# Kernel optimization log

Hardware: AMD Instinct MI355X
Metric: run time of the kernel (lower is better)

## Reference

```python
import jax, jax.numpy as jnp
import numpy as np

F_NUM, KW, EMB = 256, 2, 300


def _conv_pool(X, W, b):
    # X: [B, L, E]; W: [F, kw, E]; b: [F]. Conv2d over [kw, E] window (full embedding
    # width) -> [B, F, T], ReLU, then AvgPool over the full T -> [B, F].
    kw = W.shape[1]
    T = X.shape[1] - kw + 1
    Xs = jnp.stack([X[:, k:k + T, :] for k in range(kw)], axis=1)  # [B, kw, T, E]
    y = jnp.einsum('fke,bkte->bft', W, Xs) + b[None, :, None]
    return jax.nn.relu(y).mean(axis=2)


def _unit(v):
    return v / jnp.sqrt((v * v).sum(-1, keepdims=True))


def setup_inputs() -> dict:
    key = jax.random.key(0)
    ks = jax.random.split(key, 20)
    wscale = 1.0 / np.sqrt(KW * EMB)
    inp = {
        'mention_vec': jax.random.normal(ks[0], (256, 10, 300), jnp.float32),
        'context_vec': jax.random.normal(ks[1], (256, 20, 300), jnp.float32),
        'doc_vec': jax.random.normal(ks[2], (200, 300), jnp.float32),
        'title_vec': jax.random.normal(ks[3], (1024, 20, 300), jnp.float32),
        'body_vec': jax.random.normal(ks[4], (1024, 200, 300), jnp.float32),
        'W_ms': jax.random.normal(ks[5], (F_NUM, KW, EMB), jnp.float32) * wscale,
        'b_ms': jax.random.normal(ks[6], (F_NUM,), jnp.float32) * wscale,
        'W_mc': jax.random.normal(ks[7], (F_NUM, KW, EMB), jnp.float32) * wscale,
        'b_mc': jax.random.normal(ks[8], (F_NUM,), jnp.float32) * wscale,
        'W_md': jax.random.normal(ks[9], (F_NUM, KW, EMB), jnp.float32) * wscale,
        'b_md': jax.random.normal(ks[10], (F_NUM,), jnp.float32) * wscale,
        'W_et': jax.random.normal(ks[11], (F_NUM, KW, EMB), jnp.float32) * wscale,
        'b_et': jax.random.normal(ks[12], (F_NUM,), jnp.float32) * wscale,
        'W_eb': jax.random.normal(ks[13], (F_NUM, KW, EMB), jnp.float32) * wscale,
        'b_eb': jax.random.normal(ks[14], (F_NUM,), jnp.float32) * wscale,
        'w_local': jax.random.normal(ks[15], (6,), jnp.float32) * 0.1,
        'b_local': jax.random.normal(ks[16], (1,), jnp.float32) * 0.1,
        'mention_entity': jax.random.randint(ks[17], (256, 1024), 0, 2, jnp.int32),
    }
    return inp


def reference(mention_vec, context_vec, doc_vec, title_vec, body_vec,
              W_ms, b_ms, W_mc, b_mc, W_md, b_md, W_et, b_et, W_eb, b_eb,
              w_local, b_local, mention_entity):
    # Per-branch conv + relu + avg-pool feature extraction -> [*, F] vectors.
    ms = _conv_pool(mention_vec, W_ms, b_ms)        # [m, F]
    mc = _conv_pool(context_vec, W_mc, b_mc)        # [m, F]
    md = _conv_pool(doc_vec[None], W_md, b_md)[0]   # [F]
    et = _conv_pool(title_vec, W_et, b_et)          # [n, F]
    eb = _conv_pool(body_vec, W_eb, b_eb)           # [n, F]

    nms, nmc, net, neb, nmd = _unit(ms), _unit(mc), _unit(et), _unit(eb), _unit(md)
    cos_st = nms @ net.T                             # [m, n]
    cos_ct = nmc @ net.T
    cos_sb = nms @ neb.T
    cos_cb = nmc @ neb.T
    cos_dt = jnp.broadcast_to((net @ nmd)[None, :], cos_st.shape)
    cos_db = jnp.broadcast_to((neb @ nmd)[None, :], cos_st.shape)

    # cos(x,y)/2 + 0.5, but features are exactly 0 where mention_entity == 0.
    feats = jnp.stack([cos_st, cos_dt, cos_ct, cos_sb, cos_db, cos_cb], axis=-1)
    feats = feats / 2.0 + 0.5                        # [m, n, 6]
    mask = mention_entity.astype(feats.dtype)
    feats = feats * mask[:, :, None]

    score = feats @ w_local + b_local[0]             # [m, n] (tiny 6->1 linear)
    score = score * mask

    # masked softmax with temperature 0.1 (e**(x/0.1) * mask, row-normalized)
    e = jnp.exp(score / 0.1) * mask
    norm = e / e.sum(axis=1, keepdims=True)
    return score, norm
```

## Files before the change

kernel.cpp:

```cpp
#include <hip/hip_runtime.h>
#include <math.h>

typedef __bf16 bf16_t;
typedef __bf16 bf16x4 __attribute__((ext_vector_type(4)));
typedef __bf16 bf16x8 __attribute__((ext_vector_type(8)));
typedef float  f32x4  __attribute__((ext_vector_type(4)));

#define FNUM 256
#define KPAD 608
#define NKS  19

__global__ __launch_bounds__(256)
void prep_w_swz(const float* __restrict__ w0, const float* __restrict__ w1,
                const float* __restrict__ w2, const float* __restrict__ w3,
                const float* __restrict__ w4, bf16_t* __restrict__ wp) {
    int tg = blockIdx.x * 4 + (threadIdx.x >> 6);
    if (tg >= 1520) return;
    int l  = threadIdx.x & 63;
    int br = tg / 304;
    int rem = tg % 304;
    int ks = rem / 16, ft = rem % 16;
    const float* src;
    switch (br) {
        case 0: src = w0; break;
        case 1: src = w1; break;
        case 2: src = w2; break;
        case 3: src = w3; break;
        default: src = w4; break;
    }
    int f = ft * 16 + (l & 15);
    int k0 = ks * 32 + (l >> 4) * 8;
    bf16x8 v;
#pragma unroll
    for (int e = 0; e < 8; e++) {
        int k = k0 + e;
        v[e] = (k < 600) ? (bf16_t)src[(size_t)f * 600 + k] : (bf16_t)0.f;
    }
    *(bf16x8*)(wp + (size_t)br * FNUM * KPAD + ((size_t)(ks * 16 + ft) * 512 + (size_t)l * 8)) = v;
}

__global__ __launch_bounds__(512, 4)
void conv_body(const float* __restrict__ X, const bf16_t* __restrict__ Wswz,
               const float* __restrict__ bias, float* __restrict__ part,
               const float* __restrict__ X2, const bf16_t* __restrict__ W2,
               const float* __restrict__ bias2) {
    constexpr int NFRAG = 8;
    constexpr int TT    = 128;
    constexpr int NROWS = TT + 1;
    __shared__ bf16_t Xlds[NROWS * 300 + 8];

    const int tid = threadIdx.x;
    const int l   = tid & 63;
    const int w   = tid >> 6;
    const int g   = l >> 4;
    const int l15 = l & 15;

    const float* Xb;
    const bf16_t* Wb;
    const float* bp;
    int slot, t0;
    if ((int)blockIdx.x >= 2048) {
        int c = blockIdx.x - 2048;
        Xb = X2; Wb = W2; bp = bias2;
        slot = 2048 + c;
        t0 = c * TT;
    } else {
        int batch = blockIdx.x >> 1;
        int c = blockIdx.x & 1;
        Xb = X + (size_t)batch * 60000;
        Wb = Wswz; bp = bias;
        slot = batch * 2 + c;
        t0 = c * TT;
    }

    {
        const int vr  = (200 - t0 < NROWS) ? (200 - t0) : NROWS;
        const float* src = Xb + (size_t)t0 * 300;
        const int nF4 = vr * 75;
        for (int v = tid; v < nF4; v += 512) {
            float4 fv = *(const float4*)(src + (size_t)v * 4);
            bf16x4 hv = { (bf16_t)fv.x, (bf16_t)fv.y, (bf16_t)fv.z, (bf16_t)fv.w };
            *(bf16x4*)(Xlds + v * 4) = hv;
        }
        bf16x4 z4 = { (bf16_t)0.f, (bf16_t)0.f, (bf16_t)0.f, (bf16_t)0.f };
        for (int v = nF4 + tid; v < NROWS * 75; v += 512)
            *(bf16x4*)(Xlds + v * 4) = z4;
        if (tid < 4) ((unsigned int*)(Xlds + NROWS * 300))[tid] = 0u;
    }

    const bf16_t* wa = Wb + ((size_t)(2 * w) * 512 + (size_t)l * 8);

    int boff[NFRAG];
#pragma unroll
    for (int j = 0; j < NFRAG; j++)
        boff[j] = (j * 16 + l15) * 300 + g * 8;

    bf16x8 aCur[2], aNxt[2];
#pragma unroll
    for (int i = 0; i < 2; i++) aCur[i] = *(const bf16x8*)(wa + i * 512);

    __syncthreads();

    f32x4 acc[2][NFRAG];
#pragma unroll
    for (int i = 0; i < 2; i++)
#pragma unroll
        for (int j = 0; j < NFRAG; j++)
            acc[i][j] = (f32x4){0.f, 0.f, 0.f, 0.f};

    for (int ks = 0; ks < NKS; ++ks) {
        if (ks + 1 < NKS) {
            const bf16_t* wn_p = wa + (size_t)(ks + 1) * 16 * 512;
#pragma unroll
            for (int i = 0; i < 2; i++) aNxt[i] = *(const bf16x8*)(wn_p + i * 512);
        }
        const int k0 = ks * 32;
        bf16x8 bb[NFRAG];
#pragma unroll
        for (int j = 0; j < NFRAG; j++) {
            bf16x4 lo = *(const bf16x4*)(Xlds + boff[j] + k0);
            bf16x4 hi = *(const bf16x4*)(Xlds + boff[j] + k0 + 4);
            bb[j] = __builtin_shufflevector(lo, hi, 0, 1, 2, 3, 4, 5, 6, 7);
        }
#pragma unroll
        for (int i = 0; i < 2; i++)
#pragma unroll
            for (int j = 0; j < NFRAG; j++)
                acc[i][j] = __builtin_amdgcn_mfma_f32_16x16x32_bf16(aCur[i], bb[j], acc[i][j], 0, 0, 0);
#pragma unroll
        for (int i = 0; i < 2; i++) aCur[i] = aNxt[i];
    }

#pragma unroll
    for (int i = 0; i < 2; i++) {
#pragma unroll
        for (int r = 0; r < 4; r++) {
            const int row = w * 32 + i * 16 + g * 4 + r;
            const float bi = bp[row];
            float s = 0.f;
#pragma unroll
            for (int j = 0; j < NFRAG; j++) {
                int t = t0 + j * 16 + l15;
                float v = acc[i][j][r] + bi;
                v = fmaxf(v, 0.f);
                s += (t < 199) ? v : 0.f;
            }
            s += __shfl_xor(s, 1);
            s += __shfl_xor(s, 2);
            s += __shfl_xor(s, 4);
            s += __shfl_xor(s, 8);
            if (l15 == 0) part[(size_t)slot * 256 + row] = s;
        }
    }
}

__global__ __launch_bounds__(256)
void combine_norm(const float* __restrict__ part, float* __restrict__ nebT,
                  float* __restrict__ nmd) {
    __shared__ float red[4];
    int bid = blockIdx.x, tid = threadIdx.x;
    float v = part[((size_t)bid * 2 + 0) * 256 + tid]
            + part[((size_t)bid * 2 + 1) * 256 + tid];
    float sq = v * v;
    sq += __shfl_xor(sq, 1);
    sq += __shfl_xor(sq, 2);
    sq += __shfl_xor(sq, 4);
    sq += __shfl_xor(sq, 8);
    sq += __shfl_xor(sq, 16);
    sq += __shfl_xor(sq, 32);
    if ((tid & 63) == 0) red[tid >> 6] = sq;
    __syncthreads();
    float tot = red[0] + red[1] + red[2] + red[3];
    float o = v / sqrtf(tot);
    if (bid >= 1024) nmd[tid] = o;
    else             nebT[(size_t)tid * 1024 + bid] = o;
}

template<int NF>
__device__ __forceinline__ void kloop_s(const bf16_t* __restrict__ wa,
        const bf16_t* __restrict__ buf, f32x4 (&acc)[2][NF], const int (&boff)[NF]) {
    bf16x8 aCur[2], aNxt[2];
    aCur[0] = *(const bf16x8*)(wa);
    aCur[1] = *(const bf16x8*)(wa + 512);
#pragma unroll
    for (int ks = 0; ks < NKS; ++ks) {
        if (ks + 1 < NKS) {
            const bf16_t* wn = wa + (size_t)(ks + 1) * (16 * 512);
            aNxt[0] = *(const bf16x8*)(wn);
            aNxt[1] = *(const bf16x8*)(wn + 512);
        }
        const int k0 = ks * 32;
#pragma unroll
        for (int j = 0; j < NF; ++j) {
            const bf16_t* p = buf + boff[j] + k0;
            bf16x4 lo = *(const bf16x4*)(p);
            bf16x4 hi = *(const bf16x4*)(p + 4);
            bf16x8 bb = __builtin_shufflevector(lo, hi, 0, 1, 2, 3, 4, 5, 6, 7);
            acc[0][j] = __builtin_amdgcn_mfma_f32_16x16x32_bf16(aCur[0], bb, acc[0][j], 0, 0, 0);
            acc[1][j] = __builtin_amdgcn_mfma_f32_16x16x32_bf16(aCur[1], bb, acc[1][j], 0, 0, 0);
        }
        aCur[0] = aNxt[0]; aCur[1] = aNxt[1];
    }
}

template<int NFB, int L, int T, int BSTR, int ARRE>
__global__ __launch_bounds__(512, 4)
void conv_small(const float* __restrict__ XA, const bf16_t* __restrict__ WA,
                const float* __restrict__ bA, float* __restrict__ outA,
                const float* __restrict__ XB, const bf16_t* __restrict__ WB,
                const float* __restrict__ bB, float* __restrict__ outB,
                int nABlocks) {
    constexpr int NTOT = 4 * NFB;
    __shared__ bf16_t Xs[ARRE];
    __shared__ float feat4[4][256];

    const int tid = threadIdx.x, l = tid & 63, w = tid >> 6, g = l >> 4, l15 = l & 15;
    const bool modeA = ((int)blockIdx.x < nABlocks);
    const int grp = modeA ? (int)blockIdx.x : ((int)blockIdx.x - nABlocks);
    const int batch0 = grp * 4;
    const float* Xsrc = modeA ? XA : XB;
    const bf16_t* Wb = modeA ? WA : WB;
    const float* bp = modeA ? bA : bB;

#pragma unroll
    for (int b = 0; b < 4; ++b) {
        const float4* s4 = (const float4*)(Xsrc + (size_t)(batch0 + b) * (L * 300));
        for (int v = tid; v < L * 75; v += 512) {
            float4 f = s4[v];
            bf16x4 h = { (bf16_t)f.x, (bf16_t)f.y, (bf16_t)f.z, (bf16_t)f.w };
            *(bf16x4*)(Xs + b * BSTR + v * 4) = h;
        }
        if (tid < 2) {
            bf16x4 z = { (bf16_t)0.f, (bf16_t)0.f, (bf16_t)0.f, (bf16_t)0.f };
            *(bf16x4*)(Xs + b * BSTR + L * 300 + tid * 4) = z;
        }
    }
    __syncthreads();

    int boff[NTOT];
#pragma unroll
    for (int j = 0; j < NTOT; ++j)
        boff[j] = (j / NFB) * BSTR + ((j % NFB) * 16 + l15) * 300 + g * 8;

    f32x4 acc[2][NTOT];
#pragma unroll
    for (int a = 0; a < 2; a++)
#pragma unroll
        for (int j = 0; j < NTOT; j++) acc[a][j] = (f32x4){0.f, 0.f, 0.f, 0.f};

    const bf16_t* wa = Wb + (size_t)(2 * w) * 512 + (size_t)l * 8;
    kloop_s<NTOT>(wa, Xs, acc, boff);

#pragma unroll
    for (int jb = 0; jb < 4; ++jb) {
#pragma unroll
        for (int a = 0; a < 2; a++)
#pragma unroll
            for (int r = 0; r < 4; r++) {
                const float bi = bp[32 * w + a * 16 + g * 4 + r];
                float s = 0.f;
#pragma unroll
                for (int jf = 0; jf < NFB; ++jf) {
                    int t = jf * 16 + l15;
                    float v = acc[a][jb * NFB + jf][r] + bi;
                    v = fmaxf(v, 0.f);
                    s += (t < T) ? v : 0.f;
                }
                s += __shfl_xor(s, 1);
                s += __shfl_xor(s, 2);
                s += __shfl_xor(s, 4);
                s += __shfl_xor(s, 8);
                if (l15 == 0) feat4[jb][32 * w + a * 16 + g * 4 + r] = s;
            }
    }
    __syncthreads();

    if (w < 4) {
        float vv[4];
        float sq = 0.f;
#pragma unroll
        for (int q = 0; q < 4; q++) { vv[q] = feat4[w][l * 4 + q]; sq += vv[q] * vv[q]; }
        sq += __shfl_xor(sq, 1);
        sq += __shfl_xor(sq, 2);
        sq += __shfl_xor(sq, 4);
        sq += __shfl_xor(sq, 8);
        sq += __shfl_xor(sq, 16);
        sq += __shfl_xor(sq, 32);
        float rsq = 1.f / sqrtf(sq);
        int batch = batch0 + w;
        if (modeA) {
#pragma unroll
            for (int q = 0; q < 4; q++)
                outA[(size_t)(l * 4 + q) * 1024 + batch] = vv[q] * rsq;
        } else {
            float4 o = { vv[0] * rsq, vv[1] * rsq, vv[2] * rsq, vv[3] * rsq };
            *(float4*)(outB + (size_t)batch * 256 + l * 4) = o;
        }
    }
}

__global__ __launch_bounds__(256)
void dt_db_kernel(const float* __restrict__ nmd, const float* __restrict__ netT,
                  const float* __restrict__ nebT, float* __restrict__ dt,
                  float* __restrict__ db) {
    __shared__ float md[256];
    int tid = threadIdx.x;
    md[tid] = nmd[tid];
    __syncthreads();
    int n = blockIdx.x * 256 + tid;
    float dT = 0.f, dB = 0.f;
    for (int k = 0; k < 256; ++k) {
        float mk = md[k];
        dT += mk * netT[(size_t)k * 1024 + n];
        dB += mk * nebT[(size_t)k * 1024 + n];
    }
    dt[n] = dT;
    db[n] = dB;
}

__global__ __launch_bounds__(256)
void pair1(const float* __restrict__ nms, const float* __restrict__ nmc,
           const float* __restrict__ netT, const float* __restrict__ nebT,
           const float* __restrict__ dt, const float* __restrict__ db,
           const float* __restrict__ wl, const float* __restrict__ bl,
           const int* __restrict__ me, float* __restrict__ out,
           float* __restrict__ epart) {
    __shared__ float sA[4 * 256], sB[4 * 256];
    const int tid = threadIdx.x;
    const int mt = blockIdx.x >> 2;
    const int nt = blockIdx.x & 3;
    const int m0 = mt * 4, n0 = nt * 256;
    for (int v = tid; v < 1024; v += 256) {
        sA[v] = nms[(size_t)m0 * 256 + v];
        sB[v] = nmc[(size_t)m0 * 256 + v];
    }
    __syncthreads();
    const int ws = tid >> 6;
    const int nl = tid & 63;
    const int n  = n0 + nl * 4;
    const int m  = m0 + ws;

    float dst[4] = {0,0,0,0}, dct[4] = {0,0,0,0}, dsb[4] = {0,0,0,0}, dcb[4] = {0,0,0,0};
    for (int k = 0; k < 256; ++k) {
        float4 tv = *(const float4*)(netT + (size_t)k * 1024 + n);
        float4 bv = *(const float4*)(nebT + (size_t)k * 1024 + n);
        float a = sA[ws * 256 + k];
        float c = sB[ws * 256 + k];
        dst[0] += a * tv.x; dst[1] += a * tv.y; dst[2] += a * tv.z; dst[3] += a * tv.w;
        dct[0] += c * tv.x; dct[1] += c * tv.y; dct[2] += c * tv.z; dct[3] += c * tv.w;
        dsb[0] += a * bv.x; dsb[1] += a * bv.y; dsb[2] += a * bv.z; dsb[3] += a * bv.w;
        dcb[0] += c * bv.x; dcb[1] += c * bv.y; dcb[2] += c * bv.z; dcb[3] += c * bv.w;
    }

    float w0 = wl[0], w1 = wl[1], w2 = wl[2], w3 = wl[3], w4 = wl[4], w5 = wl[5], b = bl[0];
    float dtq[4], dbq[4];
    *(float4*)dtq = *(const float4*)(dt + n);
    *(float4*)dbq = *(const float4*)(db + n);
    const int* mp = me + (size_t)m * 1024 + n;
    float scv[4], evv[4];
    float esum = 0.f;
#pragma unroll
    for (int q = 0; q < 4; q++) {
        float msk = (float)mp[q];
        float f_st = dst[q] * 0.5f + 0.5f;
        float f_dt = dtq[q] * 0.5f + 0.5f;
        float f_ct = dct[q] * 0.5f + 0.5f;
        float f_sb = dsb[q] * 0.5f + 0.5f;
        float f_db = dbq[q] * 0.5f + 0.5f;
        float f_cb = dcb[q] * 0.5f + 0.5f;
        float s = f_st * w0 + f_dt * w1 + f_ct * w2 + f_sb * w3 + f_db * w4 + f_cb * w5 + b;
        s = (msk != 0.f) ? s : 0.f;
        scv[q] = s;
        evv[q] = (msk != 0.f) ? expf(s / 0.1f) : 0.f;
        esum += evv[q];
    }
    esum += __shfl_xor(esum, 1);
    esum += __shfl_xor(esum, 2);
    esum += __shfl_xor(esum, 4);
    esum += __shfl_xor(esum, 8);
    esum += __shfl_xor(esum, 16);
    esum += __shfl_xor(esum, 32);
    if (nl == 0) epart[(size_t)m * 4 + nt] = esum;

    *(float4*)(out + (size_t)m * 1024 + n) = *(float4*)scv;
    *(float4*)(out + 262144 + (size_t)m * 1024 + n) = *(float4*)evv;
}

__global__ __launch_bounds__(256)
void pair2(const float* __restrict__ epart, float* __restrict__ out2) {
    int m = blockIdx.x, tid = threadIdx.x;
    float tot = epart[(size_t)m * 4 + 0] + epart[(size_t)m * 4 + 1]
              + epart[(size_t)m * 4 + 2] + epart[(size_t)m * 4 + 3];
    float inv = 1.f / tot;
#pragma unroll
    for (int q = 0; q < 4; q++)
        out2[(size_t)m * 1024 + q * 256 + tid] *= inv;
}

extern "C" void kernel_launch(void* const* d_in, const int* in_sizes, int n_in,
                              void* d_out, int out_size, void* d_ws, size_t ws_size,
                              hipStream_t stream) {
    const float* mention = (const float*)d_in[0];
    const float* context = (const float*)d_in[1];
    const float* doc     = (const float*)d_in[2];
    const float* title   = (const float*)d_in[3];
    const float* body    = (const float*)d_in[4];
    const float* W_ms = (const float*)d_in[5];  const float* b_ms = (const float*)d_in[6];
    const float* W_mc = (const float*)d_in[7];  const float* b_mc = (const float*)d_in[8];
    const float* W_md = (const float*)d_in[9];  const float* b_md = (const float*)d_in[10];
    const float* W_et = (const float*)d_in[11]; const float* b_et = (const float*)d_in[12];
    const float* W_eb = (const float*)d_in[13]; const float* b_eb = (const float*)d_in[14];
    const float* w_local = (const float*)d_in[15];
    const float* b_local = (const float*)d_in[16];
    const int*   me      = (const int*)d_in[17];
    float* out = (float*)d_out;

    char* ws = (char*)d_ws;
    bf16_t* Wp = (bf16_t*)ws;
    size_t off = (size_t)5 * FNUM * KPAD * 2;
    float* part = (float*)(ws + off); off += (size_t)1025 * 2 * 256 * 4;
    float* nms  = (float*)(ws + off); off += 256 * 256 * 4;
    float* nmc  = (float*)(ws + off); off += 256 * 256 * 4;
    float* netT = (float*)(ws + off); off += 1024 * 256 * 4;
    float* nebT = (float*)(ws + off); off += 1024 * 256 * 4;
    float* nmd  = (float*)(ws + off); off += 256 * 4;
    float* dt   = (float*)(ws + off); off += 1024 * 4;
    float* db   = (float*)(ws + off); off += 1024 * 4;
    float* epart= (float*)(ws + off); off += 256 * 4 * 4;

    const bf16_t* Wms = Wp + (size_t)0 * FNUM * KPAD;
    const bf16_t* Wmc = Wp + (size_t)1 * FNUM * KPAD;
    const bf16_t* Wmd = Wp + (size_t)2 * FNUM * KPAD;
    const bf16_t* Wet = Wp + (size_t)3 * FNUM * KPAD;
    const bf16_t* Web = Wp + (size_t)4 * FNUM * KPAD;

    prep_w_swz<<<380, 256, 0, stream>>>(W_ms, W_mc, W_md, W_et, W_eb, Wp);

    conv_body<<<2050, 512, 0, stream>>>(body, Web, b_eb, part, doc, Wmd, b_md);

    conv_small<2, 20, 19, 6016, 27968><<<320, 512, 0, stream>>>(
        title, Wet, b_et, netT, context, Wmc, b_mc, nmc, 256);
    conv_small<1, 10, 9, 5120, 20480><<<64, 512, 0, stream>>>(
        mention, Wms, b_ms, netT, mention, Wms, b_ms, nms, 0);

    combine_norm<<<1025, 256, 0, stream>>>(part, nebT, nmd);
    dt_db_kernel<<<4, 256, 0, stream>>>(nmd, netT, nebT, dt, db);
    pair1<<<256, 256, 0, stream>>>(nms, nmc, netT, nebT, dt, db, w_local, b_local, me, out, epart);
    pair2<<<256, 256, 0, stream>>>(epart, out + 262144);
}
```

Measured before the change: 240.3 us.

## Fuse doc-cosine dot products into pair kernel and batch body loads

Removes the separate dt_db kernel and computes the doc-title and doc-body dot products inside pair1's existing k-loop, reusing the already-loaded netT/nebT vectors. This drops one launch and a small, poorly parallel kernel, at the cost of redundant recomputation across the m-tiles. The conv_body X staging loop now issues four float4 loads before converting, giving more memory-level parallelism. Pooled results go through shared memory so the partial sums are written with one coalesced store.

```diff
diff --git a/kernel.cpp b/kernel.cpp
--- a/kernel.cpp
+++ b/kernel.cpp
@@ -48,6 +48,7 @@
     constexpr int TT    = 128;
     constexpr int NROWS = TT + 1;
     __shared__ bf16_t Xlds[NROWS * 300 + 8];
+    __shared__ float  feat[256];
 
     const int tid = threadIdx.x;
     const int l   = tid & 63;
@@ -75,12 +76,23 @@
 
     {
         const int vr  = (200 - t0 < NROWS) ? (200 - t0) : NROWS;
-        const float* src = Xb + (size_t)t0 * 300;
+        const float4* s4 = (const float4*)(Xb + (size_t)t0 * 300);
         const int nF4 = vr * 75;
-        for (int v = tid; v < nF4; v += 512) {
-            float4 fv = *(const float4*)(src + (size_t)v * 4);
-            bf16x4 hv = { (bf16_t)fv.x, (bf16_t)fv.y, (bf16_t)fv.z, (bf16_t)fv.w };
-            *(bf16x4*)(Xlds + v * 4) = hv;
+        for (int v0 = tid; v0 < nF4; v0 += 512 * 4) {
+            float4 t[4];
+#pragma unroll
+            for (int q = 0; q < 4; ++q) {
+                int v = v0 + q * 512;
+                if (v < nF4) t[q] = s4[v];
+            }
+#pragma unroll
+            for (int q = 0; q < 4; ++q) {
+                int v = v0 + q * 512;
+                if (v < nF4) {
+                    bf16x4 hv = { (bf16_t)t[q].x, (bf16_t)t[q].y, (bf16_t)t[q].z, (bf16_t)t[q].w };
+                    *(bf16x4*)(Xlds + v * 4) = hv;
+                }
+            }
         }
         bf16x4 z4 = { (bf16_t)0.f, (bf16_t)0.f, (bf16_t)0.f, (bf16_t)0.f };
         for (int v = nF4 + tid; v < NROWS * 75; v += 512)
@@ -149,9 +161,12 @@
             s += __shfl_xor(s, 2);
             s += __shfl_xor(s, 4);
             s += __shfl_xor(s, 8);
-            if (l15 == 0) part[(size_t)slot * 256 + row] = s;
-        }
-    }
+            if (l15 == 0) feat[row] = s;
+        }
+    }
+    __syncthreads();
+    if (tid < 256)
+        part[(size_t)slot * 256 + tid] = feat[tid];
 }
 
 __global__ __launch_bounds__(256)
@@ -300,32 +315,13 @@
 }
 
 __global__ __launch_bounds__(256)
-void dt_db_kernel(const float* __restrict__ nmd, const float* __restrict__ netT,
-                  const float* __restrict__ nebT, float* __restrict__ dt,
-                  float* __restrict__ db) {
-    __shared__ float md[256];
-    int tid = threadIdx.x;
-    md[tid] = nmd[tid];
-    __syncthreads();
-    int n = blockIdx.x * 256 + tid;
-    float dT = 0.f, dB = 0.f;
-    for (int k = 0; k < 256; ++k) {
-        float mk = md[k];
-        dT += mk * netT[(size_t)k * 1024 + n];
-        dB += mk * nebT[(size_t)k * 1024 + n];
-    }
-    dt[n] = dT;
-    db[n] = dB;
-}
-
-__global__ __launch_bounds__(256)
 void pair1(const float* __restrict__ nms, const float* __restrict__ nmc,
            const float* __restrict__ netT, const float* __restrict__ nebT,
-           const float* __restrict__ dt, const float* __restrict__ db,
+           const float* __restrict__ nmd,
            const float* __restrict__ wl, const float* __restrict__ bl,
            const int* __restrict__ me, float* __restrict__ out,
            float* __restrict__ epart) {
-    __shared__ float sA[4 * 256], sB[4 * 256];
+    __shared__ float sA[4 * 256], sB[4 * 256], md[256];
     const int tid = threadIdx.x;
     const int mt = blockIdx.x >> 2;
     const int nt = blockIdx.x & 3;
@@ -334,6 +330,7 @@
         sA[v] = nms[(size_t)m0 * 256 + v];
         sB[v] = nmc[(size_t)m0 * 256 + v];
     }
+    md[tid] = nmd[tid];
     __syncthreads();
     const int ws = tid >> 6;
     const int nl = tid & 63;
@@ -341,21 +338,22 @@
     const int m  = m0 + ws;
 
     float dst[4] = {0,0,0,0}, dct[4] = {0,0,0,0}, dsb[4] = {0,0,0,0}, dcb[4] = {0,0,0,0};
+    float dtq[4] = {0,0,0,0}, dbq[4] = {0,0,0,0};
     for (int k = 0; k < 256; ++k) {
         float4 tv = *(const float4*)(netT + (size_t)k * 1024 + n);
         float4 bv = *(const float4*)(nebT + (size_t)k * 1024 + n);
         float a = sA[ws * 256 + k];
         float c = sB[ws * 256 + k];
+        float mk = md[k];
         dst[0] += a * tv.x; dst[1] += a * tv.y; dst[2] += a * tv.z; dst[3] += a * tv.w;
         dct[0] += c * tv.x; dct[1] += c * tv.y; dct[2] += c * tv.z; dct[3] += c * tv.w;
         dsb[0] += a * bv.x; dsb[1] += a * bv.y; dsb[2] += a * bv.z; dsb[3] += a * bv.w;
         dcb[0] += c * bv.x; dcb[1] += c * bv.y; dcb[2] += c * bv.z; dcb[3] += c * bv.w;
+        dtq[0] += mk * tv.x; dtq[1] += mk * tv.y; dtq[2] += mk * tv.z; dtq[3] += mk * tv.w;
+        dbq[0] += mk * bv.x; dbq[1] += mk * bv.y; dbq[2] += mk * bv.z; dbq[3] += mk * bv.w;
     }
 
     float w0 = wl[0], w1 = wl[1], w2 = wl[2], w3 = wl[3], w4 = wl[4], w5 = wl[5], b = bl[0];
-    float dtq[4], dbq[4];
-    *(float4*)dtq = *(const float4*)(dt + n);
-    *(float4*)dbq = *(const float4*)(db + n);
     const int* mp = me + (size_t)m * 1024 + n;
     float scv[4], evv[4];
     float esum = 0.f;
@@ -424,8 +422,6 @@
     float* netT = (float*)(ws + off); off += 1024 * 256 * 4;
     float* nebT = (float*)(ws + off); off += 1024 * 256 * 4;
     float* nmd  = (float*)(ws + off); off += 256 * 4;
-    float* dt   = (float*)(ws + off); off += 1024 * 4;
-    float* db   = (float*)(ws + off); off += 1024 * 4;
     float* epart= (float*)(ws + off); off += 256 * 4 * 4;
 
     const bf16_t* Wms = Wp + (size_t)0 * FNUM * KPAD;
@@ -444,7 +440,6 @@
         mention, Wms, b_ms, netT, mention, Wms, b_ms, nms, 0);
 
     combine_norm<<<1025, 256, 0, stream>>>(part, nebT, nmd);
-    dt_db_kernel<<<4, 256, 0, stream>>>(nmd, netT, nebT, dt, db);
-    pair1<<<256, 256, 0, stream>>>(nms, nmc, netT, nebT, dt, db, w_local, b_local, me, out, epart);
+    pair1<<<256, 256, 0, stream>>>(nms, nmc, netT, nebT, nmd, w_local, b_local, me, out, epart);
     pair2<<<256, 256, 0, stream>>>(epart, out + 262144);
 }
```

Result: faster. 233.8 us (-2.7%).
